# Performance work log

Hardware: AMD Instinct MI355X
Metric: run time of the kernel (lower is better)

The kernel has to match this reference:

```python
import jax, jax.numpy as jnp
import numpy as np

EPSILON = 1e-8
PSD_EPS = 1e-5


def _mask_norm(mask):
    # torch.norm(mask, inf, dim=1, keepdim=True): max |.| over F axis
    max_abs = jnp.max(jnp.abs(mask), axis=1, keepdims=True)
    return mask / (max_abs + EPSILON)


def _estimate_psd(mask, cm):
    # mask: [B,F,T] real; cm: [B,C,F,T] complex -> psd [B,F,C,C]
    x = jnp.transpose(cm, (0, 2, 1, 3))            # [B,F,C,T]
    m = mask[:, :, None, :]                        # [B,F,1,T]
    nom = jnp.einsum('bfct,bfdt->bfcd', x * m, jnp.conj(x))
    den = jnp.clip(jnp.sum(m, axis=-1, keepdims=True), PSD_EPS, None)
    psd = nom / den
    return psd + 1j * jnp.asarray(PSD_EPS, psd.real.dtype)


def setup_inputs() -> dict:
    key = jax.random.key(0)
    k1, k2, k3, k4 = jax.random.split(key, 4)
    B, C, F, T = 8, 8, 257, 1500
    return {
        'speech_mask': jax.random.uniform(k1, (B, F, T), dtype=jnp.float32),
        'noise_mask': jax.random.uniform(k2, (B, F, T), dtype=jnp.float32),
        'cm_real': jax.random.normal(k3, (B, C, F, T), dtype=jnp.float32),
        'cm_imag': jax.random.normal(k4, (B, C, F, T), dtype=jnp.float32),
    }


def reference(speech_mask, noise_mask, cm_real, cm_imag):
    eps = EPSILON
    cm = cm_real + 1j * cm_imag                    # [B,C,F,T] complex64
    B, C, F, T = cm.shape

    sm = _mask_norm(speech_mask)
    nm = _mask_norm(noise_mask)

    speech_psd = _estimate_psd(sm, cm) + 1j * jnp.float32(eps)   # [B,F,C,C]
    noise_psd = _estimate_psd(nm, cm) + 1j * jnp.float32(eps)

    # diagonal loading + inverse, stabilized
    eye = jnp.eye(C, dtype=noise_psd.dtype)
    noise_psd_inv = jnp.linalg.inv(noise_psd + eye * eps)
    noise_psd_inv = noise_psd_inv + 1j * jnp.float32(eps)

    A = noise_psd_inv @ speech_psd                 # [B,F,C,C]
    tr = jnp.einsum('bfcc->bf', A) + eps           # trace [B,F]

    ref_vec = jnp.zeros((B, C), dtype=A.dtype).at[:, 0].set(1.0)
    u = jnp.einsum('bfcd,bd->bfc', A, ref_vec)     # [B,F,C]
    weight = u / tr[..., None]                     # [B,F,C]
    w = jnp.transpose(weight, (0, 2, 1))           # [B,C,F]

    # apply beamformer: sum_c conj(w) * cm -> [B,F,T]
    out = jnp.einsum('bcf,bcft->bft', jnp.conj(w), cm)
    return jnp.stack([out.real, out.imag])         # [2,B,F,T] float32
```

## Files before the change

### kernel.cpp

```cpp
#include <hip/hip_runtime.h>

#define Bb 8
#define Cc 8
#define Ff 257
#define Tt 1500
#define P2 750
#define BF (Bb*Ff)

__device__ __forceinline__ constexpr int utIdx(int c, int d) { return c*(17-c)/2 + (d-c); }
__device__ __forceinline__ constexpr int odIdx(int c, int d) { return 7*c - c*(c-1)/2 + (d-c-1); }

constexpr float EPSv   = 1e-8f;
constexpr float PSDEPS = 1e-5f;
constexpr float IMADD  = 1e-5f + 1e-8f;

__global__ void mask_pmax(const float* __restrict__ sm, const float* __restrict__ nm,
                          float* __restrict__ pmax_s, float* __restrict__ pmax_n) {
    int t  = blockIdx.x * 256 + threadIdx.x;
    int ch = blockIdx.y;
    int b  = blockIdx.z;
    if (t >= Tt) return;
    int f0 = ch * 33, f1 = min(Ff, f0 + 33);
    float ms = 0.f, mn = 0.f;
    for (int f = f0; f < f1; ++f) {
        ms = fmaxf(ms, fabsf(sm[(b*Ff + f)*Tt + t]));
        mn = fmaxf(mn, fabsf(nm[(b*Ff + f)*Tt + t]));
    }
    pmax_s[(b*8 + ch)*Tt + t] = ms;
    pmax_n[(b*8 + ch)*Tt + t] = mn;
}

__global__ void mask_inv(const float* __restrict__ pmax_s, const float* __restrict__ pmax_n,
                         float* __restrict__ inv_s, float* __restrict__ inv_n) {
    int t = blockIdx.x * 256 + threadIdx.x;
    int b = blockIdx.y;
    if (t >= Tt) return;
    float ms = 0.f, mn = 0.f;
    #pragma unroll
    for (int ch = 0; ch < 8; ++ch) {
        ms = fmaxf(ms, pmax_s[(b*8 + ch)*Tt + t]);
        mn = fmaxf(mn, pmax_n[(b*8 + ch)*Tt + t]);
    }
    inv_s[b*Tt + t] = 1.0f / (ms + EPSv);
    inv_n[b*Tt + t] = 1.0f / (mn + EPSv);
}

__global__ __launch_bounds__(256, 3) void mvdr_main(
    const float* __restrict__ smask, const float* __restrict__ nmask,
    const float* __restrict__ cmr,   const float* __restrict__ cmi,
    const float* __restrict__ inv_s, const float* __restrict__ inv_n,
    float* __restrict__ out)
{
    const int blk = blockIdx.x;
    const int b = blk / Ff, f = blk % Ff;
    const int tid  = threadIdx.x;
    const int par  = tid & 1;
    const int pair = tid >> 1;
    const int wid  = tid >> 6;
    const int lane = tid & 63;

    const float2* sm2 = (const float2*)smask + (b*Ff + f)*P2;
    const float2* nm2 = (const float2*)nmask + (b*Ff + f)*P2;
    const float2* is2 = (const float2*)inv_s + b*P2;
    const float2* in2 = (const float2*)inv_n + b*P2;
    const float2* m2  = par ? nm2 : sm2;
    const float2* iv2 = par ? in2 : is2;
    const int cstride = Ff * P2;
    const float2* xr2 = (const float2*)cmr + (b*Cc)*cstride + f*P2;
    const float2* xi2 = (const float2*)cmi + (b*Cc)*cstride + f*P2;

    float acc[64];
    #pragma unroll
    for (int v = 0; v < 64; ++v) acc[v] = 0.f;
    float summ = 0.f;

    int p = pair;
    #pragma unroll 1
    for (int it = 0; it < 6; ++it, p += 128) {
        if (p < P2) {
            float2 mk = m2[p], iv = iv2[p];
            float2 xr[8], xi[8];
            #pragma unroll
            for (int c = 0; c < 8; ++c) { xr[c] = xr2[p + c*cstride]; xi[c] = xi2[p + c*cstride]; }
            float mx = mk.x * iv.x, my = mk.y * iv.y;
            summ += mx + my;
            #pragma unroll
            for (int c = 0; c < 8; ++c) {
                float ax = mx*xr[c].x, ay = my*xr[c].y, bx = mx*xi[c].x, by = my*xi[c].y;
                {
                    const int k = utIdx(c, c);
                    float t0 = acc[k];
                    t0 = fmaf(ax, xr[c].x, t0); t0 = fmaf(bx, xi[c].x, t0);
                    t0 = fmaf(ay, xr[c].y, t0); t0 = fmaf(by, xi[c].y, t0);
                    acc[k] = t0;
                }
                #pragma unroll
                for (int d = c + 1; d < 8; ++d) {
                    const int k = utIdx(c, d);
                    const int j = 36 + odIdx(c, d);
                    float t0 = acc[k], t1 = acc[j];
                    t0 = fmaf(ax, xr[d].x, t0); t0 = fmaf(bx, xi[d].x, t0);
                    t0 = fmaf(ay, xr[d].y, t0); t0 = fmaf(by, xi[d].y, t0);
                    t1 = fmaf(bx, xr[d].x, t1); t1 = fmaf(-ax, xi[d].x, t1);
                    t1 = fmaf(by, xr[d].y, t1); t1 = fmaf(-ay, xi[d].y, t1);
                    acc[k] = t0; acc[j] = t1;
                }
            }
        }
    }

    #pragma unroll
    for (int o = 2; o <= 32; o <<= 1) summ += __shfl_xor(summ, o, 64);
    __shared__ float msum[4], nsum[4];
    if (lane == 0) msum[wid] = summ;
    if (lane == 1) nsum[wid] = summ;

    #pragma unroll
    for (int v = 0; v < 64; ++v) {
        acc[v] += __shfl_xor(acc[v], 2, 64);
        acc[v] += __shfl_xor(acc[v], 4, 64);
    }
    __shared__ float red[64*36];
    const int col = wid*8 + (lane >> 3);
    if (par == 0 && (lane & 7) == 0) {
        #pragma unroll
        for (int v = 0; v < 64; ++v) red[v*36 + col] = acc[v];
    }
    __syncthreads();
    float Sval = 0.f;
    if (tid < 64) {
        const float4* row = (const float4*)(red + tid*36);
        #pragma unroll
        for (int k = 0; k < 8; ++k) { float4 r4 = row[k]; Sval += r4.x + r4.y + r4.z + r4.w; }
    }
    __syncthreads();
    if (par == 1 && (lane & 7) == 1) {
        #pragma unroll
        for (int v = 0; v < 64; ++v) red[v*36 + col] = acc[v];
    }
    __syncthreads();
    float Nval = 0.f;
    if (tid < 64) {
        const float4* row = (const float4*)(red + tid*36);
        #pragma unroll
        for (int k = 0; k < 8; ++k) { float4 r4 = row[k]; Nval += r4.x + r4.y + r4.z + r4.w; }
    }

    __shared__ float SreM[64], SimM[64];
    __shared__ float Are[128], Aim[128];
    __shared__ float dre[8], dim_[8], wre[8], wim[8];

    if (tid < 64) {
        const float den_s = fmaxf(msum[0]+msum[1]+msum[2]+msum[3], PSDEPS);
        const float den_n = fmaxf(nsum[0]+nsum[1]+nsum[2]+nsum[3], PSDEPS);
        int cc_, dd_;
        if (tid < 36) { int k = tid, c = 0; while (k >= 8 - c) { k -= 8 - c; ++c; } cc_ = c; dd_ = c + k; }
        else          { int k = tid - 36, c = 0; while (k >= 7 - c) { k -= 7 - c; ++c; } cc_ = c; dd_ = c + k + 1; }
        float sv = Sval / den_s, nv = Nval / den_n;
        if (tid < 36) {
            SreM[cc_*8 + dd_] = sv; SreM[dd_*8 + cc_] = sv;
            float nvd = nv + (cc_ == dd_ ? EPSv : 0.f);
            Are[cc_*16 + dd_] = nvd; Are[dd_*16 + cc_] = nvd;
            if (cc_ == dd_) { SimM[cc_*8 + cc_] = IMADD; Aim[cc_*16 + cc_] = IMADD; }
        } else {
            SimM[cc_*8 + dd_] = IMADD + sv; SimM[dd_*8 + cc_] = IMADD - sv;
            Aim[cc_*16 + dd_] = IMADD + nv; Aim[dd_*16 + cc_] = IMADD - nv;
        }
        int r = tid >> 3, j = tid & 7;
        Are[r*16 + 8 + j] = (r == j) ? 1.f : 0.f;
        Aim[r*16 + 8 + j] = 0.f;
    }
    __syncthreads();

    {
        const bool act = tid < 64;
        const int r = (tid >> 3) & 7, cA = tid & 7;
        for (int k = 0; k < 8; ++k) {
            float pr = Are[k*16 + k], pi = Aim[k*16 + k];
            float idn = 1.0f / (pr*pr + pi*pi);
            float ipr = pr*idn, ipi = -pi*idn;
            if (act && r == k) {
                float ar0 = Are[k*16 + cA],     ai0 = Aim[k*16 + cA];
                Are[k*16 + cA]     = ar0*ipr - ai0*ipi; Aim[k*16 + cA]     = ar0*ipi + ai0*ipr;
                float ar1 = Are[k*16 + cA + 8], ai1 = Aim[k*16 + cA + 8];
                Are[k*16 + cA + 8] = ar1*ipr - ai1*ipi; Aim[k*16 + cA + 8] = ar1*ipi + ai1*ipr;
            }
            __syncthreads();
            float fr = Are[r*16 + k], fi = Aim[r*16 + k];
            float p0r = Are[k*16 + cA],     p0i = Aim[k*16 + cA];
            float p1r = Are[k*16 + cA + 8], p1i = Aim[k*16 + cA + 8];
            float o0r = 0.f, o0i = 0.f, o1r = 0.f, o1i = 0.f;
            if (r != k) {
                o0r = Are[r*16 + cA]     - (fr*p0r - fi*p0i);
                o0i = Aim[r*16 + cA]     - (fr*p0i + fi*p0r);
                o1r = Are[r*16 + cA + 8] - (fr*p1r - fi*p1i);
                o1i = Aim[r*16 + cA + 8] - (fr*p1i + fi*p1r);
            }
            __syncthreads();
            if (act && r != k) {
                Are[r*16 + cA]     = o0r; Aim[r*16 + cA]     = o0i;
                Are[r*16 + cA + 8] = o1r; Aim[r*16 + cA + 8] = o1i;
            }
            __syncthreads();
        }
    }

    if (tid < 8) {
        int c = tid;
        float ur = 0.f, ui = 0.f, tr_r = 0.f, tr_i = 0.f;
        #pragma unroll
        for (int j = 0; j < 8; ++j) {
            float vr = Are[c*16 + 8 + j], vi = Aim[c*16 + 8 + j] + EPSv;
            float s0r = SreM[j*8 + 0], s0i = SimM[j*8 + 0];
            ur += vr*s0r - vi*s0i; ui += vr*s0i + vi*s0r;
            float scr = SreM[j*8 + c], sci = SimM[j*8 + c];
            tr_r += vr*scr - vi*sci; tr_i += vr*sci + vi*scr;
        }
        dre[c] = tr_r; dim_[c] = tr_i;
        wre[c] = ur;   wim[c]  = ui;
    }
    __syncthreads();
    if (tid < 8) {
        float tr_r = EPSv, tr_i = 0.f;
        #pragma unroll
        for (int j = 0; j < 8; ++j) { tr_r += dre[j]; tr_i += dim_[j]; }
        float idn = 1.0f / (tr_r*tr_r + tr_i*tr_i);
        float ur = wre[tid], ui = wim[tid];
        wre[tid] = (ur*tr_r + ui*tr_i) * idn;
        wim[tid] = (ui*tr_r - ur*tr_i) * idn;
    }
    __syncthreads();

    float wr[8], wi[8];
    #pragma unroll
    for (int c = 0; c < 8; ++c) { wr[c] = wre[c]; wi[c] = wim[c]; }

    float2* outr = (float2*)out + (b*Ff + f)*P2;
    float2* outi = (float2*)out + (Bb*Ff)*P2 + (b*Ff + f)*P2;
    for (int pp = tid; pp < P2; pp += 256) {
        float rx = 0.f, ry = 0.f, ix = 0.f, iy = 0.f;
        #pragma unroll
        for (int c = 0; c < 8; ++c) {
            float2 a  = xr2[pp + c*cstride];
            float2 bb = xi2[pp + c*cstride];
            rx += wr[c]*a.x + wi[c]*bb.x;
            ry += wr[c]*a.y + wi[c]*bb.y;
            ix += wr[c]*bb.x - wi[c]*a.x;
            iy += wr[c]*bb.y - wi[c]*a.y;
        }
        outr[pp] = make_float2(rx, ry);
        outi[pp] = make_float2(ix, iy);
    }
}

extern "C" void kernel_launch(void* const* d_in, const int* in_sizes, int n_in,
                              void* d_out, int out_size, void* d_ws, size_t ws_size,
                              hipStream_t stream) {
    const float* smask = (const float*)d_in[0];
    const float* nmask = (const float*)d_in[1];
    const float* cmr   = (const float*)d_in[2];
    const float* cmi   = (const float*)d_in[3];
    float* ws = (float*)d_ws;
    float* pmax_s = ws;
    float* pmax_n = ws + 96000;
    float* inv_s  = ws + 192000;
    float* inv_n  = ws + 204000;

    mask_pmax<<<dim3(6, 8, 8), 256, 0, stream>>>(smask, nmask, pmax_s, pmax_n);
    mask_inv <<<dim3(6, 8),    256, 0, stream>>>(pmax_s, pmax_n, inv_s, inv_n);
    mvdr_main<<<BF, 256, 0, stream>>>(smask, nmask, cmr, cmi, inv_s, inv_n, (float*)d_out);
}
```

Measured before the change: 300.5 us.

## Split PSD accumulation across wavefronts by mask and real/imag part

```diff
diff --git a/kernel.cpp b/kernel.cpp
--- a/kernel.cpp
+++ b/kernel.cpp
@@ -5,6 +5,7 @@
 #define Ff 257
 #define Tt 1500
 #define P2 750
+#define P4 375
 #define BF (Bb*Ff)
 
 __device__ __forceinline__ constexpr int utIdx(int c, int d) { return c*(17-c)/2 + (d-c); }
@@ -45,7 +46,7 @@
     inv_n[b*Tt + t] = 1.0f / (mn + EPSv);
 }
 
-__global__ __launch_bounds__(256, 3) void mvdr_main(
+__global__ __launch_bounds__(256, 4) void mvdr_main(
     const float* __restrict__ smask, const float* __restrict__ nmask,
     const float* __restrict__ cmr,   const float* __restrict__ cmi,
     const float* __restrict__ inv_s, const float* __restrict__ inv_n,
@@ -54,109 +55,113 @@
     const int blk = blockIdx.x;
     const int b = blk / Ff, f = blk % Ff;
     const int tid  = threadIdx.x;
-    const int par  = tid & 1;
-    const int pair = tid >> 1;
     const int wid  = tid >> 6;
     const int lane = tid & 63;
+    const int msel = __builtin_amdgcn_readfirstlane(wid >> 1);
+    const int part = __builtin_amdgcn_readfirstlane(wid & 1);
 
     const float2* sm2 = (const float2*)smask + (b*Ff + f)*P2;
     const float2* nm2 = (const float2*)nmask + (b*Ff + f)*P2;
     const float2* is2 = (const float2*)inv_s + b*P2;
     const float2* in2 = (const float2*)inv_n + b*P2;
-    const float2* m2  = par ? nm2 : sm2;
-    const float2* iv2 = par ? in2 : is2;
+    const float2* m2  = msel ? nm2 : sm2;
+    const float2* iv2 = msel ? in2 : is2;
     const int cstride = Ff * P2;
     const float2* xr2 = (const float2*)cmr + (b*Cc)*cstride + f*P2;
     const float2* xi2 = (const float2*)cmi + (b*Cc)*cstride + f*P2;
 
-    float acc[64];
+    float acc[36];
     #pragma unroll
-    for (int v = 0; v < 64; ++v) acc[v] = 0.f;
+    for (int v = 0; v < 36; ++v) acc[v] = 0.f;
     float summ = 0.f;
 
-    int p = pair;
-    #pragma unroll 1
-    for (int it = 0; it < 6; ++it, p += 128) {
-        if (p < P2) {
-            float2 mk = m2[p], iv = iv2[p];
-            float2 xr[8], xi[8];
-            #pragma unroll
-            for (int c = 0; c < 8; ++c) { xr[c] = xr2[p + c*cstride]; xi[c] = xi2[p + c*cstride]; }
-            float mx = mk.x * iv.x, my = mk.y * iv.y;
+    auto body = [&](int p) {
+        float2 mk = m2[p], iv = iv2[p];
+        float2 xr[8], xi[8];
+        #pragma unroll
+        for (int c = 0; c < 8; ++c) { xr[c] = xr2[p + c*cstride]; xi[c] = xi2[p + c*cstride]; }
+        float mx = mk.x * iv.x, my = mk.y * iv.y;
+        if (part == 0) {
             summ += mx + my;
             #pragma unroll
             for (int c = 0; c < 8; ++c) {
                 float ax = mx*xr[c].x, ay = my*xr[c].y, bx = mx*xi[c].x, by = my*xi[c].y;
-                {
-                    const int k = utIdx(c, c);
+                #pragma unroll
+                for (int d = c; d < 8; ++d) {
+                    const int k = utIdx(c, d);
                     float t0 = acc[k];
-                    t0 = fmaf(ax, xr[c].x, t0); t0 = fmaf(bx, xi[c].x, t0);
-                    t0 = fmaf(ay, xr[c].y, t0); t0 = fmaf(by, xi[c].y, t0);
+                    t0 = fmaf(ax, xr[d].x, t0); t0 = fmaf(bx, xi[d].x, t0);
+                    t0 = fmaf(ay, xr[d].y, t0); t0 = fmaf(by, xi[d].y, t0);
                     acc[k] = t0;
                 }
+            }
+        } else {
+            #pragma unroll
+            for (int c = 0; c < 8; ++c) {
+                float ax = mx*xr[c].x, ay = my*xr[c].y, bx = mx*xi[c].x, by = my*xi[c].y;
                 #pragma unroll
                 for (int d = c + 1; d < 8; ++d) {
-                    const int k = utIdx(c, d);
-                    const int j = 36 + odIdx(c, d);
-                    float t0 = acc[k], t1 = acc[j];
-                    t0 = fmaf(ax, xr[d].x, t0); t0 = fmaf(bx, xi[d].x, t0);
-                    t0 = fmaf(ay, xr[d].y, t0); t0 = fmaf(by, xi[d].y, t0);
+                    const int j = odIdx(c, d);
+                    float t1 = acc[j];
                     t1 = fmaf(bx, xr[d].x, t1); t1 = fmaf(-ax, xi[d].x, t1);
                     t1 = fmaf(by, xr[d].y, t1); t1 = fmaf(-ay, xi[d].y, t1);
-                    acc[k] = t0; acc[j] = t1;
+                    acc[j] = t1;
                 }
             }
         }
-    }
-
-    #pragma unroll
-    for (int o = 2; o <= 32; o <<= 1) summ += __shfl_xor(summ, o, 64);
-    __shared__ float msum[4], nsum[4];
-    if (lane == 0) msum[wid] = summ;
-    if (lane == 1) nsum[wid] = summ;
-
-    #pragma unroll
-    for (int v = 0; v < 64; ++v) {
-        acc[v] += __shfl_xor(acc[v], 2, 64);
-        acc[v] += __shfl_xor(acc[v], 4, 64);
-    }
-    __shared__ float red[64*36];
-    const int col = wid*8 + (lane >> 3);
-    if (par == 0 && (lane & 7) == 0) {
-        #pragma unroll
-        for (int v = 0; v < 64; ++v) red[v*36 + col] = acc[v];
-    }
-    __syncthreads();
-    float Sval = 0.f;
-    if (tid < 64) {
-        const float4* row = (const float4*)(red + tid*36);
-        #pragma unroll
-        for (int k = 0; k < 8; ++k) { float4 r4 = row[k]; Sval += r4.x + r4.y + r4.z + r4.w; }
-    }
-    __syncthreads();
-    if (par == 1 && (lane & 7) == 1) {
-        #pragma unroll
-        for (int v = 0; v < 64; ++v) red[v*36 + col] = acc[v];
-    }
-    __syncthreads();
-    float Nval = 0.f;
-    if (tid < 64) {
-        const float4* row = (const float4*)(red + tid*36);
-        #pragma unroll
-        for (int k = 0; k < 8; ++k) { float4 r4 = row[k]; Nval += r4.x + r4.y + r4.z + r4.w; }
-    }
+    };
+
+    int p = lane;
+    #pragma unroll 1
+    for (int it = 0; it < 11; ++it, p += 64) body(p);
+    if (p < P2) body(p);
+
+    __shared__ float Sre[36], Sim[28], Nre[36], Nim[28];
+    __shared__ float sumSN[2];
+
+    if (part == 0) {
+        #pragma unroll
+        for (int o = 1; o <= 32; o <<= 1) {
+            summ += __shfl_xor(summ, o, 64);
+            #pragma unroll
+            for (int v = 0; v < 36; ++v) acc[v] += __shfl_xor(acc[v], o, 64);
+        }
+        if (lane == 0) {
+            float* dst = msel ? Nre : Sre;
+            #pragma unroll
+            for (int v = 0; v < 36; ++v) dst[v] = acc[v];
+            sumSN[msel] = summ;
+        }
+    } else {
+        #pragma unroll
+        for (int o = 1; o <= 32; o <<= 1) {
+            #pragma unroll
+            for (int v = 0; v < 28; ++v) acc[v] += __shfl_xor(acc[v], o, 64);
+        }
+        if (lane == 0) {
+            float* dst = msel ? Nim : Sim;
+            #pragma unroll
+            for (int v = 0; v < 28; ++v) dst[v] = acc[v];
+        }
+    }
+    __syncthreads();
 
     __shared__ float SreM[64], SimM[64];
     __shared__ float Are[128], Aim[128];
     __shared__ float dre[8], dim_[8], wre[8], wim[8];
 
     if (tid < 64) {
-        const float den_s = fmaxf(msum[0]+msum[1]+msum[2]+msum[3], PSDEPS);
-        const float den_n = fmaxf(nsum[0]+nsum[1]+nsum[2]+nsum[3], PSDEPS);
+        const float den_s = fmaxf(sumSN[0], PSDEPS);
+        const float den_n = fmaxf(sumSN[1], PSDEPS);
         int cc_, dd_;
-        if (tid < 36) { int k = tid, c = 0; while (k >= 8 - c) { k -= 8 - c; ++c; } cc_ = c; dd_ = c + k; }
-        else          { int k = tid - 36, c = 0; while (k >= 7 - c) { k -= 7 - c; ++c; } cc_ = c; dd_ = c + k + 1; }
-        float sv = Sval / den_s, nv = Nval / den_n;
+        float sv, nv;
+        if (tid < 36) {
+            int k = tid, c = 0; while (k >= 8 - c) { k -= 8 - c; ++c; } cc_ = c; dd_ = c + k;
+            sv = Sre[tid] / den_s; nv = Nre[tid] / den_n;
+        } else {
+            int k = tid - 36, c = 0; while (k >= 7 - c) { k -= 7 - c; ++c; } cc_ = c; dd_ = c + k + 1;
+            sv = Sim[tid - 36] / den_s; nv = Nim[tid - 36] / den_n;
+        }
         if (tid < 36) {
             SreM[cc_*8 + dd_] = sv; SreM[dd_*8 + cc_] = sv;
             float nvd = nv + (cc_ == dd_ ? EPSv : 0.f);
@@ -235,21 +240,29 @@
     #pragma unroll
     for (int c = 0; c < 8; ++c) { wr[c] = wre[c]; wi[c] = wim[c]; }
 
-    float2* outr = (float2*)out + (b*Ff + f)*P2;
-    float2* outi = (float2*)out + (Bb*Ff)*P2 + (b*Ff + f)*P2;
-    for (int pp = tid; pp < P2; pp += 256) {
-        float rx = 0.f, ry = 0.f, ix = 0.f, iy = 0.f;
+    const int cstride4 = Ff * P4;
+    const float4* xr4 = (const float4*)xr2;
+    const float4* xi4 = (const float4*)xi2;
+    float4* outr4 = (float4*)out + (b*Ff + f)*P4;
+    float4* outi4 = (float4*)out + (Bb*Ff)*P4 + (b*Ff + f)*P4;
+    for (int pp = tid; pp < P4; pp += 256) {
+        float rx = 0.f, ry = 0.f, rz = 0.f, rw = 0.f;
+        float ix = 0.f, iy = 0.f, iz = 0.f, iw = 0.f;
         #pragma unroll
         for (int c = 0; c < 8; ++c) {
-            float2 a  = xr2[pp + c*cstride];
-            float2 bb = xi2[pp + c*cstride];
-            rx += wr[c]*a.x + wi[c]*bb.x;
-            ry += wr[c]*a.y + wi[c]*bb.y;
-            ix += wr[c]*bb.x - wi[c]*a.x;
-            iy += wr[c]*bb.y - wi[c]*a.y;
-        }
-        outr[pp] = make_float2(rx, ry);
-        outi[pp] = make_float2(ix, iy);
+            float4 a  = xr4[pp + c*cstride4];
+            float4 bb = xi4[pp + c*cstride4];
+            rx = fmaf(wr[c], a.x, fmaf(wi[c], bb.x, rx));
+            ry = fmaf(wr[c], a.y, fmaf(wi[c], bb.y, ry));
+            rz = fmaf(wr[c], a.z, fmaf(wi[c], bb.z, rz));
+            rw = fmaf(wr[c], a.w, fmaf(wi[c], bb.w, rw));
+            ix = fmaf(wr[c], bb.x, fmaf(-wi[c], a.x, ix));
+            iy = fmaf(wr[c], bb.y, fmaf(-wi[c], a.y, iy));
+            iz = fmaf(wr[c], bb.z, fmaf(-wi[c], a.z, iz));
+            iw = fmaf(wr[c], bb.w, fmaf(-wi[c], a.w, iw));
+        }
+        outr4[pp] = make_float4(rx, ry, rz, rw);
+        outi4[pp] = make_float4(ix, iy, iz, iw);
     }
 }
 
```

Result: slower. 379.6 us (+26.4%).
